# Kernel optimization log

Hardware: AMD Instinct MI355X
Metric: run time of the kernel (lower is better)

Reference implementation:

```python
import jax, jax.numpy as jnp
import numpy as np

N_NODES = 100000
N_EDGES = 1600000
D = 128
K = 3
LAMBDA_MAX = 2.0  # PyG ChebConv default for normalization='sym'


def _cheb_conv(x, row, col, w, diag, lins, bias):
    # x: [N, D]; w: [E] scaled-Laplacian off-diag weights; diag: scalar diag weight
    # lins: [K, D, D]; bias: [D]
    n = x.shape[0]

    def prop(v):
        # out[col] += w * v[row]  (sparse L_hat @ v), plus diagonal term
        return jax.ops.segment_sum(w[:, None] * v[row], col, num_segments=n) + diag * v

    Tx0 = x
    out = Tx0 @ lins[0]
    Tx1 = prop(Tx0)
    out = out + Tx1 @ lins[1]
    for k in range(2, lins.shape[0]):
        Tx2 = 2.0 * prop(Tx1) - Tx0
        out = out + Tx2 @ lins[k]
        Tx0, Tx1 = Tx1, Tx2
    return out + bias


def setup_inputs() -> dict:
    key = jax.random.key(0)
    ks = jax.random.split(key, 10)
    glorot = float(np.sqrt(6.0 / (D + D)))
    X = jax.random.normal(ks[0], (N_NODES, D), dtype=jnp.float32)
    edge_index = jax.random.randint(ks[1], (2, N_EDGES), 0, N_NODES, dtype=jnp.int64)
    edge_weight = jax.random.uniform(ks[2], (N_EDGES,), dtype=jnp.float32)
    H = jax.random.normal(ks[3], (N_NODES, D), dtype=jnp.float32)
    C = jax.random.normal(ks[4], (N_NODES, D), dtype=jnp.float32)
    # gate order: i, f, c, o
    W = jax.random.uniform(ks[5], (4, D, D), dtype=jnp.float32, minval=-glorot, maxval=glorot)
    b = jnp.zeros((4, D), dtype=jnp.float32)
    conv_W = jax.random.uniform(ks[6], (4, K, D, D), dtype=jnp.float32, minval=-glorot, maxval=glorot)
    conv_b = jnp.zeros((4, D), dtype=jnp.float32)
    return {"X": X, "edge_index": edge_index, "edge_weight": edge_weight,
            "H": H, "C": C, "W": W, "b": b, "conv_W": conv_W, "conv_b": conv_b}


def reference(X, edge_index, edge_weight, H, C, W, b, conv_W, conv_b):
    n = X.shape[0]
    row, col = edge_index[0], edge_index[1]
    # sym-normalized Laplacian, scaled: L_hat = 2L/lmax - I
    deg = jax.ops.segment_sum(edge_weight, row, num_segments=n)
    dinv = jnp.where(deg > 0, deg ** -0.5, 0.0)
    w = -(dinv[row] * edge_weight * dinv[col]) * (2.0 / LAMBDA_MAX)
    diag = 2.0 / LAMBDA_MAX - 1.0  # scalar (0.0 when lmax == 2)

    def gate(g):
        return X @ W[g] + _cheb_conv(H, row, col, w, diag, conv_W[g], conv_b[g]) + b[g]

    I = jax.nn.sigmoid(gate(0))
    F = jax.nn.sigmoid(gate(1))
    T = jnp.tanh(gate(2))
    C_new = F * C + I * T
    O = jax.nn.sigmoid(gate(3))
    H_new = O * jnp.tanh(C_new)
    return H_new
```

## Files before the change

### kernel.cpp

```cpp
#include <hip/hip_runtime.h>

#define N_NODES 100000
#define N_EDGES 1600000
#define CAP 64

typedef unsigned short ushort_t;
typedef __attribute__((ext_vector_type(8))) short bf16x8;
typedef __attribute__((ext_vector_type(4))) float f32x4;
typedef __attribute__((ext_vector_type(4))) int int4e;
typedef __attribute__((ext_vector_type(8))) unsigned short ushort8e;

__device__ __forceinline__ unsigned short f2bf(float f) {
  unsigned int u = __float_as_uint(f);
  u = (u + 0x7FFFu + ((u >> 16) & 1u)) >> 16;
  return (unsigned short)u;
}

__global__ __launch_bounds__(256) void k_misc(
    const int* __restrict__ ei, const float* __restrict__ ew,
    const float* __restrict__ X, const float* __restrict__ H,
    float* __restrict__ degc0, float* __restrict__ degc1,
    int* __restrict__ cnt, int2* __restrict__ bE,
    ushort_t* __restrict__ U,
    const float* __restrict__ W, const float* __restrict__ b,
    const float* __restrict__ cW, const float* __restrict__ cb,
    ushort_t* __restrict__ Bt, float* __restrict__ bias) {
  int bid = blockIdx.x;
  int role = bid & 7, q = bid >> 3;
  if (role < 2) {
    int e = (q * 2 + role) * 256 + threadIdx.x;
    if (e < N_EDGES) {
      float* dg = role ? degc1 : degc0;
      atomicAdd(&dg[ei[e]], ew[e]);
    }
  } else if (role < 4) {
    int e = (q * 2 + (role - 2)) * 256 + threadIdx.x;
    if (e < N_EDGES) {
      int r = ei[e], c = ei[N_EDGES + e];
      float w = ew[e];
      int pos = atomicAdd(&cnt[c], 1);
      if (pos < CAP) bE[c * CAP + pos] = make_int2(r, __float_as_int(w));
    }
  } else {
    int s = q * 4 + (role - 4);
    if (s < 12500) {
      int i = s * 256 + threadIdx.x;
      int n = i >> 5, qq = i & 31;
      float4 x = *(const float4*)(X + (size_t)n * 128 + qq * 4);
      float4 h = *(const float4*)(H + (size_t)n * 128 + qq * 4);
      ushort4 a, bb;
      a.x = f2bf(x.x); a.y = f2bf(x.y); a.z = f2bf(x.z); a.w = f2bf(x.w);
      bb.x = f2bf(h.x); bb.y = f2bf(h.y); bb.z = f2bf(h.z); bb.w = f2bf(h.w);
      *(ushort4*)(U + (size_t)n * 512 + qq * 4) = a;
      *(ushort4*)(U + (size_t)n * 512 + 128 + qq * 4) = bb;
    } else if (s < 13524) {
      int idx = (s - 12500) * 256 + threadIdx.x;
      int j = idx >> 9, k = idx & 511;
      int dd = j >> 2, g = j & 3;
      float v;
      if (k < 128) v = W[(g * 128 + k) * 128 + dd];
      else {
        int kk = k - 128;
        int blk = kk >> 7;
        v = cW[((g * 3 + blk) * 128 + (kk & 127)) * 128 + dd];
      }
      Bt[idx] = f2bf(v);
      if (k == 0) bias[j] = b[g * 128 + dd] + cb[g * 128 + dd];
    }
  }
}

__global__ __launch_bounds__(256) void k_sumdeg(
    const float* __restrict__ degc0, const float* __restrict__ degc1,
    float* __restrict__ deg) {
  int i = blockIdx.x * 256 + threadIdx.x;
  deg[i] = degc0[i] + degc1[i];
}

__global__ __launch_bounds__(256) void k_scale(
    const int* __restrict__ cnt, const float* __restrict__ deg,
    int2* __restrict__ bE) {
  int slot = blockIdx.x * 256 + threadIdx.x;
  int node = slot >> 6, i = slot & 63;
  int cn = cnt[node]; if (cn > CAP) cn = CAP;
  if (i < cn) {
    int2 p = bE[slot];
    float d = deg[p.x];
    float w = d > 0.f ? rsqrtf(d) * __int_as_float(p.y) : 0.f;
    bE[slot].y = __float_as_int(w);
  }
}

#define FMA8(A, Wt, R) { \
  A[0] = fmaf(Wt, __uint_as_float((unsigned)R.x << 16), A[0]); \
  A[1] = fmaf(Wt, __uint_as_float((unsigned)R.x & 0xffff0000u), A[1]); \
  A[2] = fmaf(Wt, __uint_as_float((unsigned)R.y << 16), A[2]); \
  A[3] = fmaf(Wt, __uint_as_float((unsigned)R.y & 0xffff0000u), A[3]); \
  A[4] = fmaf(Wt, __uint_as_float((unsigned)R.z << 16), A[4]); \
  A[5] = fmaf(Wt, __uint_as_float((unsigned)R.z & 0xffff0000u), A[5]); \
  A[6] = fmaf(Wt, __uint_as_float((unsigned)R.w << 16), A[6]); \
  A[7] = fmaf(Wt, __uint_as_float((unsigned)R.w & 0xffff0000u), A[7]); }

template <int PHASE>
__global__ __launch_bounds__(256) void k_gather(
    const int* __restrict__ cnt, const int2* __restrict__ bE,
    const float* __restrict__ deg, const float* __restrict__ H,
    ushort_t* __restrict__ U) {
  int g = threadIdx.x >> 4, lane = threadIdx.x & 15;
  int node = blockIdx.x * 16 + g;
  if (node >= N_NODES) return;
  int cn = cnt[node]; if (cn > CAP) cn = CAP;
  const int2* be = bE + node * CAP;
  const ushort_t* sb = U + (PHASE == 1 ? 128 : 256) + lane * 8;
  float dc = deg[node];
  float sc = dc > 0.f ? -rsqrtf(dc) : 0.f;

  float a0[8] = {}, a1[8] = {}, a2[8] = {}, a3[8] = {};
  float a4[8] = {}, a5[8] = {}, a6[8] = {}, a7[8] = {};
  int i = 0;
  for (; i + 8 <= cn; i += 8) {
    int4e p0 = __builtin_nontemporal_load((const int4e*)(be + i));
    int4e p1 = __builtin_nontemporal_load((const int4e*)(be + i + 2));
    int4e p2 = __builtin_nontemporal_load((const int4e*)(be + i + 4));
    int4e p3 = __builtin_nontemporal_load((const int4e*)(be + i + 6));
    int4e r0 = *(const int4e*)(sb + (size_t)p0.x * 512);
    int4e r1 = *(const int4e*)(sb + (size_t)p0.z * 512);
    int4e r2 = *(const int4e*)(sb + (size_t)p1.x * 512);
    int4e r3 = *(const int4e*)(sb + (size_t)p1.z * 512);
    int4e r4 = *(const int4e*)(sb + (size_t)p2.x * 512);
    int4e r5 = *(const int4e*)(sb + (size_t)p2.z * 512);
    int4e r6 = *(const int4e*)(sb + (size_t)p3.x * 512);
    int4e r7 = *(const int4e*)(sb + (size_t)p3.z * 512);
    FMA8(a0, __int_as_float(p0.y), r0); FMA8(a1, __int_as_float(p0.w), r1);
    FMA8(a2, __int_as_float(p1.y), r2); FMA8(a3, __int_as_float(p1.w), r3);
    FMA8(a4, __int_as_float(p2.y), r4); FMA8(a5, __int_as_float(p2.w), r5);
    FMA8(a6, __int_as_float(p3.y), r6); FMA8(a7, __int_as_float(p3.w), r7);
  }
  for (; i + 4 <= cn; i += 4) {
    int4e p0 = __builtin_nontemporal_load((const int4e*)(be + i));
    int4e p1 = __builtin_nontemporal_load((const int4e*)(be + i + 2));
    int4e r0 = *(const int4e*)(sb + (size_t)p0.x * 512);
    int4e r1 = *(const int4e*)(sb + (size_t)p0.z * 512);
    int4e r2 = *(const int4e*)(sb + (size_t)p1.x * 512);
    int4e r3 = *(const int4e*)(sb + (size_t)p1.z * 512);
    FMA8(a0, __int_as_float(p0.y), r0); FMA8(a1, __int_as_float(p0.w), r1);
    FMA8(a2, __int_as_float(p1.y), r2); FMA8(a3, __int_as_float(p1.w), r3);
  }
  for (; i < cn; ++i) {
    int2 p = be[i];
    int4e r0 = *(const int4e*)(sb + (size_t)p.x * 512);
    FMA8(a0, __int_as_float(p.y), r0);
  }
  float o[8];
#pragma unroll
  for (int j = 0; j < 8; ++j)
    o[j] = sc * (((a0[j] + a1[j]) + (a2[j] + a3[j])) +
                 ((a4[j] + a5[j]) + (a6[j] + a7[j])));

  if (PHASE == 1) {
    ushort8e u;
#pragma unroll
    for (int j = 0; j < 8; ++j) u[j] = f2bf(o[j]);
    __builtin_nontemporal_store(u, (ushort8e*)(U + (size_t)node * 512 + 256 + lane * 8));
  } else {
    float4 hlo = *(const float4*)(H + (size_t)node * 128 + lane * 8);
    float4 hhi = *(const float4*)(H + (size_t)node * 128 + lane * 8 + 4);
    ushort8e u;
    u[0] = f2bf(2.f * o[0] - hlo.x); u[1] = f2bf(2.f * o[1] - hlo.y);
    u[2] = f2bf(2.f * o[2] - hlo.z); u[3] = f2bf(2.f * o[3] - hlo.w);
    u[4] = f2bf(2.f * o[4] - hhi.x); u[5] = f2bf(2.f * o[5] - hhi.y);
    u[6] = f2bf(2.f * o[6] - hhi.z); u[7] = f2bf(2.f * o[7] - hhi.w);
    __builtin_nontemporal_store(u, (ushort8e*)(U + (size_t)node * 512 + 384 + lane * 8));
  }
}

__global__ __launch_bounds__(256) void k_gemm(
    const ushort_t* __restrict__ U, const ushort_t* __restrict__ Bt,
    const float* __restrict__ bias, const float* __restrict__ C,
    float* __restrict__ out) {
  __shared__ char ldsRaw[65536];
  char* ldsA0 = ldsRaw;
  char* ldsB0 = ldsRaw + 16384;
  char* ldsA1 = ldsRaw + 32768;
  char* ldsB1 = ldsRaw + 49152;
  float* ldsF = (float*)ldsRaw;

  const int tid = threadIdx.x;
  const int lane = tid & 63;
  const int w = tid >> 6;
  const int wr = w >> 1, wc = w & 1;
  const int b = blockIdx.x;
  const int g = (b & 7) * 391 + (b >> 3);
  const int m0 = (g >> 2) * 128;
  const int n0 = (g & 3) * 128;
  const int l15 = lane & 15;
  const int l4 = lane >> 4;

  auto stage_half = [&](int kt, char* la_base, char* lb_base, int h) {
    const int k0 = kt * 64;
#pragma unroll
    for (int is = 2 * h; is < 2 * h + 2; ++is) {
      int s = is * 256 + tid;
      int row = s >> 3;
      int cs = (s & 7) ^ (row & 7);
      const ushort_t* ga = U + (size_t)(m0 + row) * 512 + k0 + cs * 8;
      const ushort_t* gb = Bt + (size_t)(n0 + row) * 512 + k0 + cs * 8;
      char* la = la_base + (is * 256 + (tid & 192)) * 16;
      char* lb = lb_base + (is * 256 + (tid & 192)) * 16;
      __builtin_amdgcn_global_load_lds((const __attribute__((address_space(1))) void*)ga,
                                       (__attribute__((address_space(3))) void*)la, 16, 0, 0);
      __builtin_amdgcn_global_load_lds((const __attribute__((address_space(1))) void*)gb,
                                       (__attribute__((address_space(3))) void*)lb, 16, 0, 0);
    }
  };

  const int fcol = tid & 31;
  const int rbase = tid >> 5;
  float cpre[16];
#pragma unroll
  for (int half = 0; half < 2; ++half)
#pragma unroll
    for (int k = 0; k < 8; ++k) {
      int n = m0 + half * 64 + rbase + k * 8;
      int dg = (n0 >> 2) + fcol;
      cpre[half * 8 + k] = (n < N_NODES)
          ? __builtin_nontemporal_load(C + (size_t)n * 128 + dg) : 0.f;
    }

  int offA[2][4], offB[2][4];
#pragma unroll
  for (int ks = 0; ks < 2; ++ks) {
    int slot = ((ks * 4 + l4) ^ (l15 & 7)) * 16;
#pragma unroll
    for (int i = 0; i < 4; ++i) {
      offA[ks][i] = (wr * 64 + i * 16 + l15) * 128 + slot;
      offB[ks][i] = (wc * 64 + i * 16 + l15) * 128 + slot;
    }
  }

  f32x4 acc[4][4] = {};

  stage_half(0, ldsA0, ldsB0, 0);
  stage_half(0, ldsA0, ldsB0, 1);

  for (int kt = 0; kt < 8; ++kt) {
    char* curA = (kt & 1) ? ldsA1 : ldsA0;
    char* curB = (kt & 1) ? ldsB1 : ldsB0;
    char* nA = (kt & 1) ? ldsA0 : ldsA1;
    char* nB = (kt & 1) ? ldsB0 : ldsB1;
    if (kt < 7) {
      stage_half(kt + 1, nA, nB, 0);
      asm volatile("s_waitcnt vmcnt(4)" ::: "memory");
    } else {
      asm volatile("s_waitcnt vmcnt(0)" ::: "memory");
    }
    __builtin_amdgcn_s_barrier();
    __builtin_amdgcn_sched_barrier(0);

    {
      bf16x8 af[4], bfr[4];
#pragma unroll
      for (int mi = 0; mi < 4; ++mi) af[mi] = *(const bf16x8*)(curA + offA[0][mi]);
#pragma unroll
      for (int ni = 0; ni < 4; ++ni) bfr[ni] = *(const bf16x8*)(curB + offB[0][ni]);
      asm volatile("s_waitcnt lgkmcnt(0)" ::: "memory");
      __builtin_amdgcn_sched_barrier(0);
      __builtin_amdgcn_s_setprio(1);
#pragma unroll
      for (int mi = 0; mi < 4; ++mi)
#pragma unroll
        for (int ni = 0; ni < 4; ++ni)
          acc[mi][ni] = __builtin_amdgcn_mfma_f32_16x16x32_bf16(af[mi], bfr[ni], acc[mi][ni], 0, 0, 0);
      __builtin_amdgcn_s_setprio(0);
    }
    if (kt < 7) stage_half(kt + 1, nA, nB, 1);
    {
      bf16x8 af[4], bfr[4];
#pragma unroll
      for (int mi = 0; mi < 4; ++mi) af[mi] = *(const bf16x8*)(curA + offA[1][mi]);
#pragma unroll
      for (int ni = 0; ni < 4; ++ni) bfr[ni] = *(const bf16x8*)(curB + offB[1][ni]);
      asm volatile("s_waitcnt lgkmcnt(0)" ::: "memory");
      __builtin_amdgcn_sched_barrier(0);
      __builtin_amdgcn_s_setprio(1);
#pragma unroll
      for (int mi = 0; mi < 4; ++mi)
#pragma unroll
        for (int ni = 0; ni < 4; ++ni)
          acc[mi][ni] = __builtin_amdgcn_mfma_f32_16x16x32_bf16(af[mi], bfr[ni], acc[mi][ni], 0, 0, 0);
      __builtin_amdgcn_s_setprio(0);
    }
    __builtin_amdgcn_s_barrier();
  }

#pragma unroll
  for (int half = 0; half < 2; ++half) {
    if (wr == half) {
#pragma unroll
      for (int ni = 0; ni < 4; ++ni) {
        int col = wc * 64 + ni * 16 + l15;
        float bv = bias[n0 + col];
#pragma unroll
        for (int mi = 0; mi < 4; ++mi)
#pragma unroll
          for (int r = 0; r < 4; ++r)
            ldsF[(mi * 16 + l4 * 4 + r) * 132 + col] = acc[mi][ni][r] + bv;
      }
    }
    __syncthreads();
#pragma unroll
    for (int k = 0; k < 8; ++k) {
      int p = tid + k * 256;
      int rl = p >> 5, f = p & 31;
      int n = m0 + half * 64 + rl;
      if (n < N_NODES) {
        float4 pre = *(const float4*)&ldsF[rl * 132 + f * 4];
        int dg = (n0 >> 2) + f;
        float ig = __builtin_amdgcn_rcpf(1.f + __expf(-pre.x));
        float fg = __builtin_amdgcn_rcpf(1.f + __expf(-pre.y));
        float ec = __expf(-2.f * fabsf(pre.z));
        float tg = __builtin_copysignf((1.f - ec) * __builtin_amdgcn_rcpf(1.f + ec), pre.z);
        float og = __builtin_amdgcn_rcpf(1.f + __expf(-pre.w));
        float cOld = cpre[half * 8 + k];
        float cn = fg * cOld + ig * tg;
        float en = __expf(-2.f * fabsf(cn));
        float th = __builtin_copysignf((1.f - en) * __builtin_amdgcn_rcpf(1.f + en), cn);
        __builtin_nontemporal_store(og * th, out + (size_t)n * 128 + dg);
      }
    }
    __syncthreads();
  }
}

extern "C" void kernel_launch(void* const* d_in, const int* in_sizes, int n_in,
                              void* d_out, int out_size, void* d_ws, size_t ws_size,
                              hipStream_t stream) {
  const float* X  = (const float*)d_in[0];
  const int*   ei = (const int*)d_in[1];
  const float* ew = (const float*)d_in[2];
  const float* H  = (const float*)d_in[3];
  const float* C  = (const float*)d_in[4];
  const float* W  = (const float*)d_in[5];
  const float* b  = (const float*)d_in[6];
  const float* cW = (const float*)d_in[7];
  const float* cb = (const float*)d_in[8];
  float* out = (float*)d_out;
  char* ws = (char*)d_ws;

  float*    degc0 = (float*)(ws);
  float*    degc1 = (float*)(ws + 0x80000);
  float*    deg   = (float*)(ws + 0x100000);
  int*      cnt   = (int*)(ws + 0x180000);
  int2*     bE    = (int2*)(ws + 0x200000);
  ushort_t* U     = (ushort_t*)(ws + 0x3600000);
  ushort_t* Bt    = (ushort_t*)(ws + 0x9800000);
  float*    bias  = (float*)(ws + 0x9880000);

  hipMemsetAsync(ws, 0, 0x200000, stream);

  k_misc<<<27128, 256, 0, stream>>>(ei, ew, X, H, degc0, degc1, cnt, bE, U,
                                    W, b, cW, cb, Bt, bias);
  k_sumdeg<<<392, 256, 0, stream>>>(degc0, degc1, deg);
  k_scale<<<N_NODES * CAP / 256, 256, 0, stream>>>(cnt, deg, bE);
  k_gather<1><<<(N_NODES + 15) / 16, 256, 0, stream>>>(cnt, bE, deg, H, U);
  k_gather<2><<<(N_NODES + 15) / 16, 256, 0, stream>>>(cnt, bE, deg, H, U);
  k_gemm<<<3128, 256, 0, stream>>>(U, Bt, bias, C, out);
}
```

Measured before the change: 424.3 us.

## Use 8-wave GEMM blocks and drop split degree buffers

The GEMM kernel moves from 256 to 512 threads per block with 8 waves, each computing a 32x64 sub-tile instead of 64x64. Each thread now issues one staging load per half instead of two, and the epilogue is rewritten for the new thread count. This is meant to add more waves for latency hiding and cut per-thread register pressure. Separately, the degree accumulation now writes straight to a single buffer, which removes the k_sumdeg kernel launch and shrinks the memset, at the cost of more atomic contention on one array.

```diff
diff --git a/kernel.cpp b/kernel.cpp
--- a/kernel.cpp
+++ b/kernel.cpp
@@ -19,8 +19,7 @@
 __global__ __launch_bounds__(256) void k_misc(
     const int* __restrict__ ei, const float* __restrict__ ew,
     const float* __restrict__ X, const float* __restrict__ H,
-    float* __restrict__ degc0, float* __restrict__ degc1,
-    int* __restrict__ cnt, int2* __restrict__ bE,
+    float* __restrict__ deg, int* __restrict__ cnt, int2* __restrict__ bE,
     ushort_t* __restrict__ U,
     const float* __restrict__ W, const float* __restrict__ b,
     const float* __restrict__ cW, const float* __restrict__ cb,
@@ -29,10 +28,7 @@
   int role = bid & 7, q = bid >> 3;
   if (role < 2) {
     int e = (q * 2 + role) * 256 + threadIdx.x;
-    if (e < N_EDGES) {
-      float* dg = role ? degc1 : degc0;
-      atomicAdd(&dg[ei[e]], ew[e]);
-    }
+    if (e < N_EDGES) atomicAdd(&deg[ei[e]], ew[e]);
   } else if (role < 4) {
     int e = (q * 2 + (role - 2)) * 256 + threadIdx.x;
     if (e < N_EDGES) {
@@ -70,13 +66,6 @@
   }
 }
 
-__global__ __launch_bounds__(256) void k_sumdeg(
-    const float* __restrict__ degc0, const float* __restrict__ degc1,
-    float* __restrict__ deg) {
-  int i = blockIdx.x * 256 + threadIdx.x;
-  deg[i] = degc0[i] + degc1[i];
-}
-
 __global__ __launch_bounds__(256) void k_scale(
     const int* __restrict__ cnt, const float* __restrict__ deg,
     int2* __restrict__ bE) {
@@ -174,7 +163,7 @@
   }
 }
 
-__global__ __launch_bounds__(256) void k_gemm(
+__global__ __launch_bounds__(512, 4) void k_gemm(
     const ushort_t* __restrict__ U, const ushort_t* __restrict__ Bt,
     const float* __restrict__ bias, const float* __restrict__ C,
     float* __restrict__ out) {
@@ -198,47 +187,45 @@
 
   auto stage_half = [&](int kt, char* la_base, char* lb_base, int h) {
     const int k0 = kt * 64;
-#pragma unroll
-    for (int is = 2 * h; is < 2 * h + 2; ++is) {
-      int s = is * 256 + tid;
-      int row = s >> 3;
-      int cs = (s & 7) ^ (row & 7);
-      const ushort_t* ga = U + (size_t)(m0 + row) * 512 + k0 + cs * 8;
-      const ushort_t* gb = Bt + (size_t)(n0 + row) * 512 + k0 + cs * 8;
-      char* la = la_base + (is * 256 + (tid & 192)) * 16;
-      char* lb = lb_base + (is * 256 + (tid & 192)) * 16;
-      __builtin_amdgcn_global_load_lds((const __attribute__((address_space(1))) void*)ga,
-                                       (__attribute__((address_space(3))) void*)la, 16, 0, 0);
-      __builtin_amdgcn_global_load_lds((const __attribute__((address_space(1))) void*)gb,
-                                       (__attribute__((address_space(3))) void*)lb, 16, 0, 0);
-    }
+    int s = h * 512 + tid;
+    int row = s >> 3;
+    int cs = (s & 7) ^ (row & 7);
+    const ushort_t* ga = U + (size_t)(m0 + row) * 512 + k0 + cs * 8;
+    const ushort_t* gb = Bt + (size_t)(n0 + row) * 512 + k0 + cs * 8;
+    char* la = la_base + (h * 512 + (tid & 448)) * 16;
+    char* lb = lb_base + (h * 512 + (tid & 448)) * 16;
+    __builtin_amdgcn_global_load_lds((const __attribute__((address_space(1))) void*)ga,
+                                     (__attribute__((address_space(3))) void*)la, 16, 0, 0);
+    __builtin_amdgcn_global_load_lds((const __attribute__((address_space(1))) void*)gb,
+                                     (__attribute__((address_space(3))) void*)lb, 16, 0, 0);
   };
 
   const int fcol = tid & 31;
   const int rbase = tid >> 5;
-  float cpre[16];
+  float cpre[8];
 #pragma unroll
   for (int half = 0; half < 2; ++half)
 #pragma unroll
-    for (int k = 0; k < 8; ++k) {
-      int n = m0 + half * 64 + rbase + k * 8;
+    for (int k = 0; k < 4; ++k) {
+      int n = m0 + half * 64 + rbase + k * 16;
       int dg = (n0 >> 2) + fcol;
-      cpre[half * 8 + k] = (n < N_NODES)
+      cpre[half * 4 + k] = (n < N_NODES)
           ? __builtin_nontemporal_load(C + (size_t)n * 128 + dg) : 0.f;
     }
 
-  int offA[2][4], offB[2][4];
+  int offA[2][2], offB[2][4];
 #pragma unroll
   for (int ks = 0; ks < 2; ++ks) {
     int slot = ((ks * 4 + l4) ^ (l15 & 7)) * 16;
 #pragma unroll
-    for (int i = 0; i < 4; ++i) {
-      offA[ks][i] = (wr * 64 + i * 16 + l15) * 128 + slot;
+    for (int i = 0; i < 2; ++i)
+      offA[ks][i] = (wr * 32 + i * 16 + l15) * 128 + slot;
+#pragma unroll
+    for (int i = 0; i < 4; ++i)
       offB[ks][i] = (wc * 64 + i * 16 + l15) * 128 + slot;
-    }
-  }
-
-  f32x4 acc[4][4] = {};
+  }
+
+  f32x4 acc[2][4] = {};
 
   stage_half(0, ldsA0, ldsB0, 0);
   stage_half(0, ldsA0, ldsB0, 1);
@@ -250,7 +237,7 @@
     char* nB = (kt & 1) ? ldsB0 : ldsB1;
     if (kt < 7) {
       stage_half(kt + 1, nA, nB, 0);
-      asm volatile("s_waitcnt vmcnt(4)" ::: "memory");
+      asm volatile("s_waitcnt vmcnt(2)" ::: "memory");
     } else {
       asm volatile("s_waitcnt vmcnt(0)" ::: "memory");
     }
@@ -258,16 +245,16 @@
     __builtin_amdgcn_sched_barrier(0);
 
     {
-      bf16x8 af[4], bfr[4];
-#pragma unroll
-      for (int mi = 0; mi < 4; ++mi) af[mi] = *(const bf16x8*)(curA + offA[0][mi]);
+      bf16x8 af[2], bfr[4];
+#pragma unroll
+      for (int mi = 0; mi < 2; ++mi) af[mi] = *(const bf16x8*)(curA + offA[0][mi]);
 #pragma unroll
       for (int ni = 0; ni < 4; ++ni) bfr[ni] = *(const bf16x8*)(curB + offB[0][ni]);
       asm volatile("s_waitcnt lgkmcnt(0)" ::: "memory");
       __builtin_amdgcn_sched_barrier(0);
       __builtin_amdgcn_s_setprio(1);
 #pragma unroll
-      for (int mi = 0; mi < 4; ++mi)
+      for (int mi = 0; mi < 2; ++mi)
 #pragma unroll
         for (int ni = 0; ni < 4; ++ni)
           acc[mi][ni] = __builtin_amdgcn_mfma_f32_16x16x32_bf16(af[mi], bfr[ni], acc[mi][ni], 0, 0, 0);
@@ -275,16 +262,16 @@
     }
     if (kt < 7) stage_half(kt + 1, nA, nB, 1);
     {
-      bf16x8 af[4], bfr[4];
-#pragma unroll
-      for (int mi = 0; mi < 4; ++mi) af[mi] = *(const bf16x8*)(curA + offA[1][mi]);
+      bf16x8 af[2], bfr[4];
+#pragma unroll
+      for (int mi = 0; mi < 2; ++mi) af[mi] = *(const bf16x8*)(curA + offA[1][mi]);
 #pragma unroll
       for (int ni = 0; ni < 4; ++ni) bfr[ni] = *(const bf16x8*)(curB + offB[1][ni]);
       asm volatile("s_waitcnt lgkmcnt(0)" ::: "memory");
       __builtin_amdgcn_sched_barrier(0);
       __builtin_amdgcn_s_setprio(1);
 #pragma unroll
-      for (int mi = 0; mi < 4; ++mi)
+      for (int mi = 0; mi < 2; ++mi)
 #pragma unroll
         for (int ni = 0; ni < 4; ++ni)
           acc[mi][ni] = __builtin_amdgcn_mfma_f32_16x16x32_bf16(af[mi], bfr[ni], acc[mi][ni], 0, 0, 0);
@@ -295,22 +282,22 @@
 
 #pragma unroll
   for (int half = 0; half < 2; ++half) {
-    if (wr == half) {
+    if ((wr >> 1) == half) {
 #pragma unroll
       for (int ni = 0; ni < 4; ++ni) {
         int col = wc * 64 + ni * 16 + l15;
         float bv = bias[n0 + col];
 #pragma unroll
-        for (int mi = 0; mi < 4; ++mi)
+        for (int mi = 0; mi < 2; ++mi)
 #pragma unroll
           for (int r = 0; r < 4; ++r)
-            ldsF[(mi * 16 + l4 * 4 + r) * 132 + col] = acc[mi][ni][r] + bv;
+            ldsF[((wr & 1) * 32 + mi * 16 + l4 * 4 + r) * 132 + col] = acc[mi][ni][r] + bv;
       }
     }
     __syncthreads();
 #pragma unroll
-    for (int k = 0; k < 8; ++k) {
-      int p = tid + k * 256;
+    for (int k = 0; k < 4; ++k) {
+      int p = tid + k * 512;
       int rl = p >> 5, f = p & 31;
       int n = m0 + half * 64 + rl;
       if (n < N_NODES) {
@@ -321,7 +308,7 @@
         float ec = __expf(-2.f * fabsf(pre.z));
         float tg = __builtin_copysignf((1.f - ec) * __builtin_amdgcn_rcpf(1.f + ec), pre.z);
         float og = __builtin_amdgcn_rcpf(1.f + __expf(-pre.w));
-        float cOld = cpre[half * 8 + k];
+        float cOld = cpre[half * 4 + k];
         float cn = fg * cOld + ig * tg;
         float en = __expf(-2.f * fabsf(cn));
         float th = __builtin_copysignf((1.f - en) * __builtin_amdgcn_rcpf(1.f + en), cn);
@@ -347,22 +334,18 @@
   float* out = (float*)d_out;
   char* ws = (char*)d_ws;
 
-  float*    degc0 = (float*)(ws);
-  float*    degc1 = (float*)(ws + 0x80000);
-  float*    deg   = (float*)(ws + 0x100000);
-  int*      cnt   = (int*)(ws + 0x180000);
-  int2*     bE    = (int2*)(ws + 0x200000);
-  ushort_t* U     = (ushort_t*)(ws + 0x3600000);
-  ushort_t* Bt    = (ushort_t*)(ws + 0x9800000);
-  float*    bias  = (float*)(ws + 0x9880000);
-
-  hipMemsetAsync(ws, 0, 0x200000, stream);
-
-  k_misc<<<27128, 256, 0, stream>>>(ei, ew, X, H, degc0, degc1, cnt, bE, U,
-                                    W, b, cW, cb, Bt, bias);
-  k_sumdeg<<<392, 256, 0, stream>>>(degc0, degc1, deg);
+  float*    deg  = (float*)(ws);
+  int*      cnt  = (int*)(ws + 0x80000);
+  int2*     bE   = (int2*)(ws + 0x100000);
+  ushort_t* U    = (ushort_t*)(ws + 0x3500000);
+  ushort_t* Bt   = (ushort_t*)(ws + 0x9700000);
+  float*    bias = (float*)(ws + 0x9780000);
+
+  hipMemsetAsync(ws, 0, 0x100000, stream);
+
+  k_misc<<<27128, 256, 0, stream>>>(ei, ew, X, H, deg, cnt, bE, U, W, b, cW, cb, Bt, bias);
   k_scale<<<N_NODES * CAP / 256, 256, 0, stream>>>(cnt, deg, bE);
   k_gather<1><<<(N_NODES + 15) / 16, 256, 0, stream>>>(cnt, bE, deg, H, U);
   k_gather<2><<<(N_NODES + 15) / 16, 256, 0, stream>>>(cnt, bE, deg, H, U);
-  k_gemm<<<3128, 256, 0, stream>>>(U, Bt, bias, C, out);
-}
+  k_gemm<<<3128, 512, 0, stream>>>(U, Bt, bias, C, out);
+}
```

Result: faster. 404.5 us, median of 2 (-4.7%).
